# Kernel optimization log

Hardware: AMD Instinct MI355X
Metric: run time of the kernel (lower is better)

Reference implementation:

```python
import jax, jax.numpy as jnp
import numpy as np

B, N, D, H, L = 2, 1024, 256, 4, 6
DH = D // H          # head dim 64
RDIM = DH // 2       # AxialRotaryEmbedding dim = 32 -> output feature size DH
THETA = 0.01


def setup_inputs() -> dict:
    key = jax.random.key(0)
    ks = iter(jax.random.split(key, 80))
    def nrm(shape, s=1.0):
        return jax.random.normal(next(ks), shape, jnp.float32) * s
    size = jnp.array([1024.0, 768.0], jnp.float32)
    inp = {
        'kpts0': jax.random.uniform(next(ks), (B, N, 2), jnp.float32) * size,
        'kpts1': jax.random.uniform(next(ks), (B, N, 2), jnp.float32) * size,
        'desc0': nrm((B, N, D)),
        'desc1': nrm((B, N, D)),
        'fx': 1.0 / (THETA ** (jnp.arange(0, RDIM, 2, dtype=jnp.float32) / RDIM)),
        'fy': 1.0 / (THETA ** (jnp.arange(0, RDIM, 2, dtype=jnp.float32) / RDIM)),
    }
    s = D ** -0.5
    for p in ('s', 'c'):
        inp[f'{p}_Wqk'] = nrm((L, D, D), s); inp[f'{p}_bqk'] = jnp.zeros((L, D))
        inp[f'{p}_Wv'] = nrm((L, D, D), s);  inp[f'{p}_bv'] = jnp.zeros((L, D))
        inp[f'{p}_Wo'] = nrm((L, D, D), s);  inp[f'{p}_bo'] = jnp.zeros((L, D))
        inp[f'{p}_W1'] = nrm((L, 2 * D, 2 * D), (2 * D) ** -0.5); inp[f'{p}_b1'] = jnp.zeros((L, 2 * D))
        inp[f'{p}_g'] = jnp.ones((L, 2 * D)); inp[f'{p}_be'] = jnp.zeros((L, 2 * D))
        inp[f'{p}_W2'] = nrm((L, 2 * D, D), (2 * D) ** -0.5); inp[f'{p}_b2'] = jnp.zeros((L, D))
    inp['Wp'] = nrm((D, D), s); inp['bp'] = jnp.zeros((D,))
    inp['Wm'] = nrm((D, 1), s); inp['bm'] = jnp.zeros((1,))
    return inp


def reference(kpts0, kpts1, desc0, desc1, fx, fy,
              s_Wqk, s_bqk, s_Wv, s_bv, s_Wo, s_bo, s_W1, s_b1, s_g, s_be, s_W2, s_b2,
              c_Wqk, c_bqk, c_Wv, c_bv, c_Wo, c_bo, c_W1, c_b1, c_g, c_be, c_W2, c_b2,
              Wp, bp, Wm, bm):
    size = jnp.array([1024.0, 768.0], jnp.float32)
    norm_k = lambda k: (k - size / 2) / (size.max() / 2)
    heads = lambda t: t.reshape(t.shape[0], t.shape[1], H, DH)

    def rope(pos):  # pos [B,N,2] -> cos,sin [B,N,1,DH]
        f = jnp.concatenate([jnp.repeat(pos[..., 0:1] * fx, 2, -1),
                             jnp.repeat(pos[..., 1:2] * fy, 2, -1)], -1)[:, :, None, :]
        return jnp.cos(f), jnp.sin(f)

    def rot_half(x):  # pairs (x0,x1) -> (-x1,x0)
        return jnp.stack([-x[..., 1::2], x[..., 0::2]], -1).reshape(x.shape)

    def ln(x, g, b):
        mu = x.mean(-1, keepdims=True)
        v = ((x - mu) ** 2).mean(-1, keepdims=True)
        return (x - mu) / jnp.sqrt(v + 1e-5) * g + b

    def ffn(x, m, W1, b1, g, be, W2, b2):  # x + MLP(LN(concat(x,m)))
        h = jnp.concatenate([x, m], -1) @ W1 + b1
        return x + jax.nn.gelu(ln(h, g, be), approximate=False) @ W2 + b2

    cs0, sn0 = rope(norm_k(kpts0))
    cs1, sn1 = rope(norm_k(kpts1))
    x0, x1 = desc0, desc1
    for i in range(L):
        def self_blk(x, cs, sn):  # rotary self-attention, shared qk projection
            qk = heads(x @ s_Wqk[i] + s_bqk[i])
            qr = qk * cs + rot_half(qk) * sn
            v = heads(x @ s_Wv[i] + s_bv[i])
            a = jax.nn.softmax(jnp.einsum('bnhd,bmhd->bhnm', qr, qr) * DH ** -0.5, -1)
            m = jnp.einsum('bhnm,bmhd->bnhd', a, v).reshape(x.shape) @ s_Wo[i] + s_bo[i]
            return ffn(x, m, s_W1[i], s_b1[i], s_g[i], s_be[i], s_W2[i], s_b2[i])
        x0 = self_blk(x0, cs0, sn0)
        x1 = self_blk(x1, cs1, sn1)
        # bidirectional cross-attention (CrossTransformer math path)
        sc = (DH ** -0.5) ** 0.5
        qk0 = heads(x0 @ c_Wqk[i] + c_bqk[i]) * sc
        qk1 = heads(x1 @ c_Wqk[i] + c_bqk[i]) * sc
        v0 = heads(x0 @ c_Wv[i] + c_bv[i])
        v1 = heads(x1 @ c_Wv[i] + c_bv[i])
        sim = jnp.einsum('bnhd,bmhd->bhnm', qk0, qk1)
        m0 = jnp.einsum('bhnm,bmhd->bnhd', jax.nn.softmax(sim, -1), v1).reshape(x0.shape) @ c_Wo[i] + c_bo[i]
        m1 = jnp.einsum('bhnm,bnhd->bmhd', jax.nn.softmax(sim, 2), v0).reshape(x1.shape) @ c_Wo[i] + c_bo[i]
        x0 = ffn(x0, m0, c_W1[i], c_b1[i], c_g[i], c_be[i], c_W2[i], c_b2[i])
        x1 = ffn(x1, m1, c_W1[i], c_b1[i], c_g[i], c_be[i], c_W2[i], c_b2[i])
    # MatchAssignment: sigmoid log double softmax (temp=None, use_sqrt=False -> r=1)
    md0 = (x0 @ Wp + bp) / D ** 0.25
    md1 = (x1 @ Wp + bp) / D ** 0.25
    sim = jnp.einsum('bmd,bnd->bmn', md0, md1)
    z0 = x0 @ Wm + bm  # [B,N,1]
    z1 = x1 @ Wm + bm
    cert = jax.nn.log_sigmoid(z0) + jnp.swapaxes(jax.nn.log_sigmoid(z1), 1, 2)
    core = jax.nn.log_softmax(sim, -1) + jax.nn.log_softmax(sim, 1) + cert
    scores = jnp.zeros((sim.shape[0], N + 1, N + 1), sim.dtype)
    scores = scores.at[:, :N, :N].set(core)
    scores = scores.at[:, :N, N].set(jax.nn.log_sigmoid(-z0[..., 0]))
    scores = scores.at[:, N, :N].set(jax.nn.log_sigmoid(-z1[..., 0]))
    return scores
```

## Files before the change

### kernel.cpp

```cpp
#include <hip/hip_runtime.h>
#include <hip/hip_bf16.h>
#include <math.h>

#define NB 2
#define NN 1024
#define ND 256
#define NHD 4
#define NL 6
#define NP (NN + 1)

typedef unsigned short u16;
typedef __attribute__((ext_vector_type(8))) short bf16x8;
typedef __attribute__((ext_vector_type(4))) float f32x4;

__device__ __forceinline__ u16 f2b(float f) {
    union { float f; unsigned u; } v; v.f = f;
    unsigned r = v.u + 0x7FFFu + ((v.u >> 16) & 1u);
    return (u16)(r >> 16);
}
__device__ __forceinline__ float b2f(u16 b) {
    union { unsigned u; float f; } v; v.u = ((unsigned)b) << 16;
    return v.f;
}
__device__ __forceinline__ float logsigf(float x) {
    return (x >= 0.f) ? -log1pf(expf(-x)) : (x - log1pf(expf(x)));
}

__global__ void rope_cs_kernel(const float* __restrict__ kpts, const float* __restrict__ fx,
                               const float* __restrict__ fy, float* __restrict__ cs,
                               float* __restrict__ sn) {
    int idx = blockIdx.x * 256 + threadIdx.x;
    int row = idx >> 6, j = idx & 63;
    float kx = kpts[row * 2], ky = kpts[row * 2 + 1];
    float f;
    if (j < 32) f = ((kx - 512.f) * (1.f / 512.f)) * fx[j >> 1];
    else        f = ((ky - 384.f) * (1.f / 512.f)) * fy[(j - 32) >> 1];
    cs[idx] = cosf(f);
    sn[idx] = sinf(f);
}

__global__ void copyconv_kernel(const float* __restrict__ in, float* __restrict__ outf,
                                u16* __restrict__ outb, int n) {
    int i = blockIdx.x * 256 + threadIdx.x;
    if (i < n) { float v = in[i]; outf[i] = v; outb[i] = f2b(v); }
}

__global__ void wconv_kernel(const float* __restrict__ in, u16* __restrict__ out, int K, int N,
                             size_t outZ) {
    __shared__ float t[32][33];
    int z = blockIdx.z;
    int k0 = blockIdx.y * 32, n0 = blockIdx.x * 32;
    const float* W = in + (size_t)z * K * N;
    u16* Wt = out + (size_t)z * outZ;
    int tx = threadIdx.x, ty = threadIdx.y;
    for (int i = 0; i < 32; i += 8)
        t[ty + i][tx] = W[(size_t)(k0 + ty + i) * N + n0 + tx];
    __syncthreads();
    for (int i = 0; i < 32; i += 8)
        Wt[(size_t)(n0 + ty + i) * K + k0 + tx] = f2b(t[tx][ty + i]);
}

__global__ void biaspack_kernel(const float* __restrict__ b0, const float* __restrict__ b1,
                                float* __restrict__ out, int L) {
    int idx = blockIdx.x * 256 + threadIdx.x;
    if (idx >= L * 512) return;
    int i = idx >> 9, c = idx & 511;
    out[idx] = (c < 256) ? b0[i * 256 + c] : b1[i * 256 + c - 256];
}

__global__ __launch_bounds__(256)
void gemm_mfma(const u16* __restrict__ A, const u16* __restrict__ A2,
               const u16* __restrict__ Bt, const float* __restrict__ bias,
               const float* __restrict__ res, float* __restrict__ Cf, u16* __restrict__ Cb,
               int M, int N, int K, float scale_lo, float scale_hi,
               const float* __restrict__ csp, const float* __restrict__ snp) {
    __shared__ u16 As[2][64 * 72];
    __shared__ u16 Bs[2][64 * 72];
    int tid = threadIdx.x;
    int lane = tid & 63, wave = tid >> 6;
    int row0 = blockIdx.y * 64, col0 = blockIdx.x * 64;
    int wm = (wave >> 1) * 32, wn = (wave & 1) * 32;
    int l15 = lane & 15, l4 = lane >> 4;
    f32x4 acc[2][2] = {};
    int srl = tid >> 3, sc8 = (tid & 7) * 8;

    auto loadA = [&](int k0, int it) -> bf16x8 {
        int rr = row0 + srl + it * 32;
        int kg = k0 + sc8;
        const u16* src;
        if (A2) src = (kg < 256) ? &A[(size_t)rr * 256 + kg] : &A2[(size_t)rr * 256 + kg - 256];
        else    src = &A[(size_t)rr * K + kg];
        return *(const bf16x8*)src;
    };
    auto loadB = [&](int k0, int it) -> bf16x8 {
        return *(const bf16x8*)&Bt[(size_t)(col0 + srl + it * 32) * K + k0 + sc8];
    };

    bf16x8 rA0 = loadA(0, 0), rA1 = loadA(0, 1);
    bf16x8 rB0 = loadB(0, 0), rB1 = loadB(0, 1);
    *(bf16x8*)&As[0][srl * 72 + sc8] = rA0;
    *(bf16x8*)&As[0][(srl + 32) * 72 + sc8] = rA1;
    *(bf16x8*)&Bs[0][srl * 72 + sc8] = rB0;
    *(bf16x8*)&Bs[0][(srl + 32) * 72 + sc8] = rB1;
    __syncthreads();

    int nt = K >> 6;
    for (int t = 0; t < nt; ++t) {
        int buf = t & 1;
        bool more = (t + 1) < nt;
        if (more) {
            rA0 = loadA((t + 1) * 64, 0); rA1 = loadA((t + 1) * 64, 1);
            rB0 = loadB((t + 1) * 64, 0); rB1 = loadB((t + 1) * 64, 1);
        }
#pragma unroll
        for (int ks = 0; ks < 2; ++ks) {
            bf16x8 a0 = *(bf16x8*)&As[buf][(wm + l15) * 72 + ks * 32 + l4 * 8];
            bf16x8 a1 = *(bf16x8*)&As[buf][(wm + 16 + l15) * 72 + ks * 32 + l4 * 8];
            bf16x8 b0 = *(bf16x8*)&Bs[buf][(wn + l15) * 72 + ks * 32 + l4 * 8];
            bf16x8 b1 = *(bf16x8*)&Bs[buf][(wn + 16 + l15) * 72 + ks * 32 + l4 * 8];
            acc[0][0] = __builtin_amdgcn_mfma_f32_16x16x32_bf16(a0, b0, acc[0][0], 0, 0, 0);
            acc[0][1] = __builtin_amdgcn_mfma_f32_16x16x32_bf16(a0, b1, acc[0][1], 0, 0, 0);
            acc[1][0] = __builtin_amdgcn_mfma_f32_16x16x32_bf16(a1, b0, acc[1][0], 0, 0, 0);
            acc[1][1] = __builtin_amdgcn_mfma_f32_16x16x32_bf16(a1, b1, acc[1][1], 0, 0, 0);
        }
        if (more) {
            int nb = buf ^ 1;
            *(bf16x8*)&As[nb][srl * 72 + sc8] = rA0;
            *(bf16x8*)&As[nb][(srl + 32) * 72 + sc8] = rA1;
            *(bf16x8*)&Bs[nb][srl * 72 + sc8] = rB0;
            *(bf16x8*)&Bs[nb][(srl + 32) * 72 + sc8] = rB1;
        }
        __syncthreads();
    }
#pragma unroll
    for (int mi = 0; mi < 2; ++mi)
#pragma unroll
        for (int ni = 0; ni < 2; ++ni)
#pragma unroll
            for (int j = 0; j < 4; ++j) {
                int r = row0 + wm + mi * 16 + l4 * 4 + j;
                int c = col0 + wn + ni * 16 + l15;
                float v = acc[mi][ni][j] + (bias ? bias[c] : 0.f);
                float pn = __shfl_xor(v, 1);
                if (csp && c < 256) {
                    float cc = csp[(size_t)r * 64 + (c & 63)];
                    float ss = snp[(size_t)r * 64 + (c & 63)];
                    v = (c & 1) ? (v * cc + pn * ss) : (v * cc - pn * ss);
                }
                v *= (c < 256) ? scale_lo : scale_hi;
                if (res) v += res[(size_t)r * N + c];
                if (Cf) Cf[(size_t)r * N + c] = v;
                if (Cb) Cb[(size_t)r * N + c] = f2b(v);
            }
}

#define QSTR 72
#define VDSTR 1032
#define VBUFE (4 * VDSTR)

__global__ __launch_bounds__(256)
void flash_kernel(const u16* __restrict__ Qp, const u16* __restrict__ Vp,
                  u16* __restrict__ Ob, int kswap) {
    __shared__ u16 Qs[64 * QSTR];
    __shared__ u16 Ks[2][64 * QSTR];
    __shared__ u16 Vs[2][VBUFE];
    __shared__ u16 Ps[64 * QSTR];
    int y = blockIdx.y;
    int t = y >> 3, b = (y >> 2) & 1, h = y & 3;
    int qR = t * 2048 + b * 1024;
    int kt = kswap ? (1 - t) : t;
    int kR = kt * 2048 + b * 1024;
    int i0 = blockIdx.x * 64;
    int tid = threadIdx.x, lane = tid & 63, wave = tid >> 6;
    int l15 = lane & 15, l4 = lane >> 4;
    int wm = wave * 16;
    int srl = tid >> 3, sc8 = (tid & 7) * 8;

    const u16* Qbase = Qp + (size_t)(qR + i0) * 512 + h * 64;
    const u16* Kbase = Qp + (size_t)kR * 512 + h * 64;
    const u16* Vbase = Vp + (size_t)kR * 512 + h * 64;

#pragma unroll
    for (int it = 0; it < 2; ++it) {
        int rr = srl + it * 32;
        *(bf16x8*)&Qs[rr * QSTR + sc8] = *(const bf16x8*)&Qbase[(size_t)rr * 512 + sc8];
        *(bf16x8*)&Ks[0][rr * QSTR + sc8] = *(const bf16x8*)&Kbase[(size_t)rr * 512 + sc8];
        bf16x8 v = *(const bf16x8*)&Vbase[(size_t)rr * 512 + sc8];
        *(bf16x8*)&Vs[0][(sc8 >> 4) * VDSTR + rr * 16 + (sc8 & 15)] = v;
    }
    __syncthreads();

    float m[4], l[4];
    f32x4 accO[4] = {};
#pragma unroll
    for (int j = 0; j < 4; ++j) { m[j] = -1e30f; l[j] = 0.f; }

    for (int j0 = 0; j0 < NN; j0 += 64) {
        int buf = (j0 >> 6) & 1;
        bool more = (j0 + 64) < NN;
        bf16x8 nK0, nK1, nV0, nV1;
        if (more) {
            nK0 = *(const bf16x8*)&Kbase[(size_t)(j0 + 64 + srl) * 512 + sc8];
            nK1 = *(const bf16x8*)&Kbase[(size_t)(j0 + 96 + srl) * 512 + sc8];
            nV0 = *(const bf16x8*)&Vbase[(size_t)(j0 + 64 + srl) * 512 + sc8];
            nV1 = *(const bf16x8*)&Vbase[(size_t)(j0 + 96 + srl) * 512 + sc8];
        }
        f32x4 accS[4] = {};
#pragma unroll
        for (int ks = 0; ks < 2; ++ks) {
            bf16x8 a = *(bf16x8*)&Qs[(wm + l15) * QSTR + ks * 32 + l4 * 8];
#pragma unroll
            for (int n = 0; n < 4; ++n) {
                bf16x8 bb = *(bf16x8*)&Ks[buf][(n * 16 + l15) * QSTR + ks * 32 + l4 * 8];
                accS[n] = __builtin_amdgcn_mfma_f32_16x16x32_bf16(a, bb, accS[n], 0, 0, 0);
            }
        }
        float p[4][4];
#pragma unroll
        for (int j = 0; j < 4; ++j) {
            float tm = fmaxf(fmaxf(accS[0][j], accS[1][j]), fmaxf(accS[2][j], accS[3][j]));
#pragma unroll
            for (int d = 1; d < 16; d <<= 1) tm = fmaxf(tm, __shfl_xor(tm, d));
            float mnew = fmaxf(m[j], tm);
            float rr = __expf(m[j] - mnew);
            float ts = 0.f;
#pragma unroll
            for (int n = 0; n < 4; ++n) {
                float pv = __expf(accS[n][j] - mnew);
                p[n][j] = pv; ts += pv;
            }
#pragma unroll
            for (int d = 1; d < 16; d <<= 1) ts += __shfl_xor(ts, d);
            l[j] = l[j] * rr + ts;
            m[j] = mnew;
#pragma unroll
            for (int n = 0; n < 4; ++n) accO[n][j] *= rr;
        }
#pragma unroll
        for (int n = 0; n < 4; ++n) {
            int kv = n * 16 + l15;
            int c = (kv & 32) + (((kv >> 2) & 3) << 3) + (((kv >> 4) & 1) << 2) + (kv & 3);
#pragma unroll
            for (int j = 0; j < 4; ++j)
                Ps[(wm + l4 * 4 + j) * QSTR + c] = f2b(p[n][j]);
        }
#pragma unroll
        for (int ks = 0; ks < 2; ++ks) {
            bf16x8 a = *(bf16x8*)&Ps[(wm + l15) * QSTR + ks * 32 + l4 * 8];
#pragma unroll
            for (int n = 0; n < 4; ++n) {
                unsigned va = (unsigned)(size_t)(&Vs[buf][n * VDSTR]) + ks * 1024 + lane * 8;
                unsigned long long q0, q1;
                asm volatile("ds_read_b64_tr_b16 %0, %2\n\t"
                             "ds_read_b64_tr_b16 %1, %2 offset:512\n\t"
                             "s_waitcnt lgkmcnt(0)"
                             : "=&v"(q0), "=&v"(q1) : "v"(va) : "memory");
                union { unsigned long long q[2]; bf16x8 v; } uu;
                uu.q[0] = q0; uu.q[1] = q1;
                accO[n] = __builtin_amdgcn_mfma_f32_16x16x32_bf16(a, uu.v, accO[n], 0, 0, 0);
            }
        }
        if (more) {
            int nb = buf ^ 1;
            *(bf16x8*)&Ks[nb][srl * QSTR + sc8] = nK0;
            *(bf16x8*)&Ks[nb][(srl + 32) * QSTR + sc8] = nK1;
            *(bf16x8*)&Vs[nb][(sc8 >> 4) * VDSTR + srl * 16 + (sc8 & 15)] = nV0;
            *(bf16x8*)&Vs[nb][(sc8 >> 4) * VDSTR + (srl + 32) * 16 + (sc8 & 15)] = nV1;
        }
        __syncthreads();
    }
#pragma unroll
    for (int n = 0; n < 4; ++n)
#pragma unroll
        for (int j = 0; j < 4; ++j) {
            int r = i0 + wm + l4 * 4 + j;
            int d = n * 16 + l15;
            Ob[(size_t)(qR + r) * ND + h * 64 + d] = f2b(accO[n][j] / l[j]);
        }
}

__global__ void rowstats_kernel(const float* __restrict__ S, float* __restrict__ rm,
                                float* __restrict__ rs, int ncols) {
    __shared__ float sb[256];
    int row = blockIdx.x, tid = threadIdx.x;
    const float* p = S + (size_t)row * ncols;
    float m = -1e30f;
    for (int j = tid; j < ncols; j += 256) m = fmaxf(m, p[j]);
    sb[tid] = m; __syncthreads();
    for (int s = 128; s > 0; s >>= 1) { if (tid < s) sb[tid] = fmaxf(sb[tid], sb[tid + s]); __syncthreads(); }
    m = sb[0]; __syncthreads();
    float s = 0;
    for (int j = tid; j < ncols; j += 256) s += __expf(p[j] - m);
    sb[tid] = s; __syncthreads();
    for (int st = 128; st > 0; st >>= 1) { if (tid < st) sb[tid] += sb[tid + st]; __syncthreads(); }
    if (tid == 0) { rm[row] = m; rs[row] = sb[0]; }
}

#define CSCH 8
__global__ void colstats_part(const float* __restrict__ S, float* __restrict__ pm,
                              float* __restrict__ ps) {
    int mat = blockIdx.z;
    int j = blockIdx.x * 256 + threadIdx.x;
    int r0 = blockIdx.y * (NN / CSCH);
    const float* p = S + (size_t)mat * NN * NN + (size_t)r0 * NN + j;
    float m = -1e30f;
    for (int i = 0; i < NN / CSCH; ++i) m = fmaxf(m, p[(size_t)i * NN]);
    float s = 0;
    for (int i = 0; i < NN / CSCH; ++i) s += __expf(p[(size_t)i * NN] - m);
    int o = (mat * CSCH + blockIdx.y) * NN + j;
    pm[o] = m; ps[o] = s;
}
__global__ void colstats_red(const float* __restrict__ pm, const float* __restrict__ ps,
                             float* __restrict__ cm, float* __restrict__ cs) {
    int idx = blockIdx.x * 256 + threadIdx.x;
    int mat = idx >> 10, j = idx & 1023;
    float m = -1e30f;
#pragma unroll
    for (int k = 0; k < CSCH; ++k) m = fmaxf(m, pm[(mat * CSCH + k) * NN + j]);
    float s = 0;
#pragma unroll
    for (int k = 0; k < CSCH; ++k)
        s += ps[(mat * CSCH + k) * NN + j] * __expf(pm[(mat * CSCH + k) * NN + j] - m);
    cm[idx] = m; cs[idx] = s;
}

__global__ void ln_gelu_b(const u16* __restrict__ hb, const float* __restrict__ g,
                          const float* __restrict__ be, u16* __restrict__ out) {
    __shared__ float sb[256];
    int row = blockIdx.x, tid = threadIdx.x;
    const u16* p = hb + (size_t)row * 512;
    float x0 = b2f(p[tid]), x1 = b2f(p[tid + 256]);
    sb[tid] = x0 + x1; __syncthreads();
    for (int s = 128; s > 0; s >>= 1) { if (tid < s) sb[tid] += sb[tid + s]; __syncthreads(); }
    float mu = sb[0] * (1.f / 512.f); __syncthreads();
    float d0 = x0 - mu, d1 = x1 - mu;
    sb[tid] = d0 * d0 + d1 * d1; __syncthreads();
    for (int s = 128; s > 0; s >>= 1) { if (tid < s) sb[tid] += sb[tid + s]; __syncthreads(); }
    float rstd = rsqrtf(sb[0] * (1.f / 512.f) + 1e-5f);
    float y0 = d0 * rstd * g[tid] + be[tid];
    float y1 = d1 * rstd * g[tid + 256] + be[tid + 256];
    out[(size_t)row * 512 + tid]       = f2b(0.5f * y0 * (1.f + erff(y0 * 0.70710678118654752f)));
    out[(size_t)row * 512 + tid + 256] = f2b(0.5f * y1 * (1.f + erff(y1 * 0.70710678118654752f)));
}

__global__ void zproj_kernel(const float* __restrict__ X, const float* __restrict__ Wm,
                             const float* __restrict__ bm, float* __restrict__ z) {
    __shared__ float sb[256];
    int row = blockIdx.x, tid = threadIdx.x;
    float v = X[(size_t)row * 256 + tid] * Wm[tid];
    sb[tid] = v; __syncthreads();
    for (int s = 128; s > 0; s >>= 1) { if (tid < s) sb[tid] += sb[tid + s]; __syncthreads(); }
    if (tid == 0) z[row] = sb[0] + bm[0];
}

__global__ void assemble_kernel(const float* __restrict__ sim2, const float* __restrict__ z0,
                                const float* __restrict__ z1, const float* __restrict__ rm,
                                const float* __restrict__ rs, const float* __restrict__ cm,
                                const float* __restrict__ cs, float* __restrict__ out) {
    int idx = blockIdx.x * 256 + threadIdx.x;
    if (idx >= NB * NP * NP) return;
    int b = idx / (NP * NP);
    int rem = idx - b * NP * NP;
    int i = rem / NP, j = rem - i * NP;
    float v;
    if (i < NN && j < NN) {
        float s = sim2[((size_t)b * NN + i) * NN + j];
        float lr = s - rm[b * NN + i] - logf(rs[b * NN + i]);
        float lc = s - cm[b * NN + j] - logf(cs[b * NN + j]);
        v = lr + lc + logsigf(z0[b * NN + i]) + logsigf(z1[b * NN + j]);
    } else if (i < NN) {
        v = logsigf(-z0[b * NN + i]);
    } else if (j < NN) {
        v = logsigf(-z1[b * NN + j]);
    } else {
        v = 0.f;
    }
    out[idx] = v;
}

extern "C" void kernel_launch(void* const* d_in, const int* in_sizes, int n_in,
                              void* d_out, int out_size, void* d_ws, size_t ws_size,
                              hipStream_t stream) {
    auto in = [&](int i) { return (const float*)d_in[i]; };
    const float* kpts0 = in(0);
    const float* kpts1 = in(1);
    const float* desc0 = in(2);
    const float* desc1 = in(3);
    const float* fx = in(4);
    const float* fy = in(5);
    const float* sWqk = in(6);  const float* sbqk = in(7);
    const float* sWv  = in(8);  const float* sbv  = in(9);
    const float* sWo  = in(10); const float* sbo  = in(11);
    const float* sW1  = in(12); const float* sb1  = in(13);
    const float* sg   = in(14); const float* sbe  = in(15);
    const float* sW2  = in(16); const float* sb2  = in(17);
    const float* cWqk = in(18); const float* cbqk = in(19);
    const float* cWv  = in(20); const float* cbv  = in(21);
    const float* cWo  = in(22); const float* cbo  = in(23);
    const float* cW1  = in(24); const float* cb1  = in(25);
    const float* cg   = in(26); const float* cbe  = in(27);
    const float* cW2  = in(28); const float* cb2  = in(29);
    const float* Wp = in(30); const float* bp = in(31);
    const float* Wm = in(32); const float* bm = in(33);

    const int Mst = 2 * NB * NN;
    const size_t SND = (size_t)Mst * ND;

    char* base = (char*)d_ws;
    size_t off = 0;
    auto allocf = [&](size_t n) { float* p = (float*)(base + off); off += ((n * 4 + 255) & ~(size_t)255); return p; };
    auto allocb = [&](size_t n) { u16* p = (u16*)(base + off);   off += ((n * 2 + 255) & ~(size_t)255); return p; };

    float* x    = allocf(SND);
    float* cst  = allocf((size_t)Mst * 64);
    float* snt  = allocf((size_t)Mst * 64);
    float* simb = allocf((size_t)NB * NN * NN);
    float* z    = allocf(Mst);
    float* st0  = allocf(2048);
    float* st1  = allocf(2048);
    float* st2  = allocf(2048);
    float* st3  = allocf(2048);
    float* pm   = allocf((size_t)NB * CSCH * NN);
    float* ps   = allocf((size_t)NB * CSCH * NN);
    float* bqvs = allocf((size_t)NL * 512);
    float* bqvc = allocf((size_t)NL * 512);

    u16* xb    = allocb(SND);
    u16* tQVb  = allocb((size_t)Mst * 512);
    u16* attnb = allocb(SND);
    u16* mb    = allocb(SND);
    u16* hb    = allocb((size_t)Mst * 512);
    u16* hgb   = allocb((size_t)Mst * 512);
    u16* wsqv = allocb((size_t)NL * 512 * 256);
    u16* wso  = allocb((size_t)NL * 256 * 256);
    u16* wsw1 = allocb((size_t)NL * 512 * 512);
    u16* wsw2 = allocb((size_t)NL * 512 * 256);
    u16* wcqv = allocb((size_t)NL * 512 * 256);
    u16* wco  = allocb((size_t)NL * 256 * 256);
    u16* wcw1 = allocb((size_t)NL * 512 * 512);
    u16* wcw2 = allocb((size_t)NL * 512 * 256);
    u16* wpb  = allocb((size_t)256 * 256);

    auto wconv = [&](const float* w, u16* wt, int K, int N, int Lz, size_t outZ) {
        wconv_kernel<<<dim3(N / 32, K / 32, Lz), dim3(32, 8), 0, stream>>>(w, wt, K, N, outZ);
    };
    wconv(sWqk, wsqv,             256, 256, NL, 512 * 256);
    wconv(sWv,  wsqv + 256 * 256, 256, 256, NL, 512 * 256);
    wconv(cWqk, wcqv,             256, 256, NL, 512 * 256);
    wconv(cWv,  wcqv + 256 * 256, 256, 256, NL, 512 * 256);
    wconv(sWo, wso, 256, 256, NL, 256 * 256);
    wconv(cWo, wco, 256, 256, NL, 256 * 256);
    wconv(sW1, wsw1, 512, 512, NL, 512 * 512);
    wconv(cW1, wcw1, 512, 512, NL, 512 * 512);
    wconv(sW2, wsw2, 512, 256, NL, 512 * 256);
    wconv(cW2, wcw2, 512, 256, NL, 512 * 256);
    wconv(Wp, wpb, 256, 256, 1, 256 * 256);
    biaspack_kernel<<<(NL * 512 + 255) / 256, 256, 0, stream>>>(sbqk, sbv, bqvs, NL);
    biaspack_kernel<<<(NL * 512 + 255) / 256, 256, 0, stream>>>(cbqk, cbv, bqvc, NL);

    rope_cs_kernel<<<512, 256, 0, stream>>>(kpts0, fx, fy, cst, snt);
    rope_cs_kernel<<<512, 256, 0, stream>>>(kpts1, fx, fy, cst + 2048 * 64, snt + 2048 * 64);
    copyconv_kernel<<<2048, 256, 0, stream>>>(desc0, x, xb, (int)(SND / 2));
    copyconv_kernel<<<2048, 256, 0, stream>>>(desc1, x + SND / 2, xb + SND / 2, (int)(SND / 2));

    auto gemm = [&](const u16* A, const u16* A2, const u16* Bt, const float* bias,
                    const float* res, float* Cf, u16* Cb, int M, int N, int K,
                    float slo, float shi, const float* csp, const float* snp) {
        gemm_mfma<<<dim3(N / 64, M / 64), 256, 0, stream>>>(A, A2, Bt, bias, res, Cf, Cb,
                                                            M, N, K, slo, shi, csp, snp);
    };

    const float sc = 0.35355339059327379f;

    for (int i = 0; i < NL; ++i) {
        const size_t oQV = (size_t)i * 512 * 256;
        const size_t oDD = (size_t)i * 256 * 256;
        const size_t oW1 = (size_t)i * 512 * 512;
        const size_t oW2 = (size_t)i * 512 * 256;

        gemm(xb, nullptr, wsqv + oQV, bqvs + i * 512, nullptr, nullptr, tQVb,
             Mst, 512, 256, sc, 1.f, cst, snt);
        flash_kernel<<<dim3(16, 16), 256, 0, stream>>>(tQVb, tQVb + 256, attnb, 0);
        gemm(attnb, nullptr, wso + oDD, sbo + i * ND, nullptr, nullptr, mb,
             Mst, 256, 256, 1.f, 1.f, nullptr, nullptr);
        gemm(xb, mb, wsw1 + oW1, sb1 + i * 512, nullptr, nullptr, hb,
             Mst, 512, 512, 1.f, 1.f, nullptr, nullptr);
        ln_gelu_b<<<Mst, 256, 0, stream>>>(hb, sg + i * 512, sbe + i * 512, hgb);
        gemm(hgb, nullptr, wsw2 + oW2, sb2 + i * ND, x, x, xb,
             Mst, 256, 512, 1.f, 1.f, nullptr, nullptr);

        gemm(xb, nullptr, wcqv + oQV, bqvc + i * 512, nullptr, nullptr, tQVb,
             Mst, 512, 256, sc, 1.f, nullptr, nullptr);
        flash_kernel<<<dim3(16, 16), 256, 0, stream>>>(tQVb, tQVb + 256, attnb, 1);
        gemm(attnb, nullptr, wco + oDD, cbo + i * ND, nullptr, nullptr, mb,
             Mst, 256, 256, 1.f, 1.f, nullptr, nullptr);
        gemm(xb, mb, wcw1 + oW1, cb1 + i * 512, nullptr, nullptr, hb,
             Mst, 512, 512, 1.f, 1.f, nullptr, nullptr);
        ln_gelu_b<<<Mst, 256, 0, stream>>>(hb, cg + i * 512, cbe + i * 512, hgb);
        gemm(hgb, nullptr, wcw2 + oW2, cb2 + i * ND, x, x, xb,
             Mst, 256, 512, 1.f, 1.f, nullptr, nullptr);
    }

    gemm(xb, nullptr, wpb, bp, nullptr, nullptr, attnb,
         Mst, 256, 256, 0.25f, 0.25f, nullptr, nullptr);
    zproj_kernel<<<Mst, 256, 0, stream>>>(x, Wm, bm, z);
    for (int b = 0; b < NB; ++b) {
        gemm(attnb + (size_t)b * 1024 * 256, nullptr,
             attnb + (size_t)(2048 + b * 1024) * 256, nullptr, nullptr,
             simb + (size_t)b * NN * NN, nullptr,
             1024, 1024, 256, 1.f, 1.f, nullptr, nullptr);
    }
    rowstats_kernel<<<NB * NN, 256, 0, stream>>>(simb, st0, st1, NN);
    colstats_part<<<dim3(NN / 256, CSCH, NB), 256, 0, stream>>>(simb, pm, ps);
    colstats_red<<<(NB * NN) / 256, 256, 0, stream>>>(pm, ps, st2, st3);
    int total = NB * NP * NP;
    assemble_kernel<<<(total + 255) / 256, 256, 0, stream>>>(simb, z, z + 2048, st0, st1,
                                                             st2, st3, (float*)d_out);
}
```

Measured before the change: 1.185 ms.

## Split-K flash attention merged in O-proj GEMM, fuse LN+GELU into W2 GEMM

Flash attention now splits the key dimension into two halves, giving twice as many blocks, and writes unnormalized fp32 partial outputs plus per-row max and sum. The output-projection GEMM combines the two partials while loading its A operand. LayerNorm+GELU is folded into the W2 GEMM: per-row statistics are computed in the prologue and the activation is applied as each A tile is staged. Q fragments are hoisted into registers, and the weight-conversion, rope and copy setup kernels are merged into fewer launches. The trade-offs are extra fp32 partial traffic and redundant LN/GELU work in each column block of the W2 GEMM.

```diff
diff --git a/kernel.cpp b/kernel.cpp
--- a/kernel.cpp
+++ b/kernel.cpp
@@ -5,7 +5,6 @@
 #define NB 2
 #define NN 1024
 #define ND 256
-#define NHD 4
 #define NL 6
 #define NP (NN + 1)
 
@@ -26,12 +25,13 @@
     return (x >= 0.f) ? -log1pf(expf(-x)) : (x - log1pf(expf(x)));
 }
 
-__global__ void rope_cs_kernel(const float* __restrict__ kpts, const float* __restrict__ fx,
-                               const float* __restrict__ fy, float* __restrict__ cs,
-                               float* __restrict__ sn) {
+__global__ void rope_cs_kernel(const float* __restrict__ k0p, const float* __restrict__ k1p,
+                               const float* __restrict__ fx, const float* __restrict__ fy,
+                               float* __restrict__ cs, float* __restrict__ sn) {
     int idx = blockIdx.x * 256 + threadIdx.x;
     int row = idx >> 6, j = idx & 63;
-    float kx = kpts[row * 2], ky = kpts[row * 2 + 1];
+    const float* kp = (row < 2048) ? k0p + (size_t)row * 2 : k1p + (size_t)(row - 2048) * 2;
+    float kx = kp[0], ky = kp[1];
     float f;
     if (j < 32) f = ((kx - 512.f) * (1.f / 512.f)) * fx[j >> 1];
     else        f = ((ky - 384.f) * (1.f / 512.f)) * fy[(j - 32) >> 1];
@@ -39,19 +39,25 @@
     sn[idx] = sinf(f);
 }
 
-__global__ void copyconv_kernel(const float* __restrict__ in, float* __restrict__ outf,
-                                u16* __restrict__ outb, int n) {
+__global__ void copyconv_kernel(const float* __restrict__ d0, const float* __restrict__ d1,
+                                float* __restrict__ outf, u16* __restrict__ outb) {
     int i = blockIdx.x * 256 + threadIdx.x;
-    if (i < n) { float v = in[i]; outf[i] = v; outb[i] = f2b(v); }
-}
-
-__global__ void wconv_kernel(const float* __restrict__ in, u16* __restrict__ out, int K, int N,
-                             size_t outZ) {
+    float v = (i < 524288) ? d0[i] : d1[i - 524288];
+    outf[i] = v; outb[i] = f2b(v);
+}
+
+struct WP6 {
+    const float* s[6];
+    u16* d[6];
+    unsigned long long oz[6];
+};
+__global__ void wconvM_kernel(WP6 w, int perT, int K, int N) {
     __shared__ float t[32][33];
     int z = blockIdx.z;
+    int p = z / perT, l = z - p * perT;
+    const float* W = w.s[p] + (size_t)l * K * N;
+    u16* Wt = w.d[p] + (size_t)l * w.oz[p];
     int k0 = blockIdx.y * 32, n0 = blockIdx.x * 32;
-    const float* W = in + (size_t)z * K * N;
-    u16* Wt = out + (size_t)z * outZ;
     int tx = threadIdx.x, ty = threadIdx.y;
     for (int i = 0; i < 32; i += 8)
         t[ty + i][tx] = W[(size_t)(k0 + ty + i) * N + n0 + tx];
@@ -154,22 +160,219 @@
             }
 }
 
+__global__ __launch_bounds__(256)
+void gemm_oproj(const float* __restrict__ Op, const float* __restrict__ mp,
+                const float* __restrict__ lp, const u16* __restrict__ Bt,
+                const float* __restrict__ bias, u16* __restrict__ Cb) {
+    __shared__ u16 As[2][64 * 72];
+    __shared__ u16 Bs[2][64 * 72];
+    const int N = 256, K = 256;
+    int tid = threadIdx.x;
+    int lane = tid & 63, wave = tid >> 6;
+    int row0 = blockIdx.y * 64, col0 = blockIdx.x * 64;
+    int wm = (wave >> 1) * 32, wn = (wave & 1) * 32;
+    int l15 = lane & 15, l4 = lane >> 4;
+    f32x4 acc[2][2] = {};
+    int srl = tid >> 3, sc8 = (tid & 7) * 8;
+
+    auto loadA = [&](int k0, int it) -> bf16x8 {
+        int rg = row0 + srl + it * 32;
+        int kg = k0 + sc8;
+        int h = kg >> 6, d0 = kg & 63;
+        int t = rg >> 11, bb = (rg >> 10) & 1, iq = rg & 1023;
+        int y = t * 8 + bb * 4 + h;
+        int ri = y * 1024 + iq;
+        size_t base0 = (size_t)ri * 64 + d0;
+        size_t base1 = base0 + (size_t)16384 * 64;
+        f32x4 a0 = *(const f32x4*)&Op[base0];
+        f32x4 a1 = *(const f32x4*)&Op[base0 + 4];
+        f32x4 c0 = *(const f32x4*)&Op[base1];
+        f32x4 c1 = *(const f32x4*)&Op[base1 + 4];
+        float m0 = mp[ri], m1 = mp[16384 + ri];
+        float l0 = lp[ri], l1 = lp[16384 + ri];
+        float mf = fmaxf(m0, m1);
+        float e0 = __expf(m0 - mf), e1 = __expf(m1 - mf);
+        float inv = 1.f / (l0 * e0 + l1 * e1);
+        e0 *= inv; e1 *= inv;
+        u16 o[8];
+#pragma unroll
+        for (int e = 0; e < 4; ++e) {
+            o[e] = f2b(a0[e] * e0 + c0[e] * e1);
+            o[4 + e] = f2b(a1[e] * e0 + c1[e] * e1);
+        }
+        return *(bf16x8*)o;
+    };
+    auto loadB = [&](int k0, int it) -> bf16x8 {
+        return *(const bf16x8*)&Bt[(size_t)(col0 + srl + it * 32) * K + k0 + sc8];
+    };
+
+    bf16x8 rA0 = loadA(0, 0), rA1 = loadA(0, 1);
+    bf16x8 rB0 = loadB(0, 0), rB1 = loadB(0, 1);
+    *(bf16x8*)&As[0][srl * 72 + sc8] = rA0;
+    *(bf16x8*)&As[0][(srl + 32) * 72 + sc8] = rA1;
+    *(bf16x8*)&Bs[0][srl * 72 + sc8] = rB0;
+    *(bf16x8*)&Bs[0][(srl + 32) * 72 + sc8] = rB1;
+    __syncthreads();
+
+    for (int t = 0; t < 4; ++t) {
+        int buf = t & 1;
+        bool more = (t + 1) < 4;
+        if (more) {
+            rA0 = loadA((t + 1) * 64, 0); rA1 = loadA((t + 1) * 64, 1);
+            rB0 = loadB((t + 1) * 64, 0); rB1 = loadB((t + 1) * 64, 1);
+        }
+#pragma unroll
+        for (int ks = 0; ks < 2; ++ks) {
+            bf16x8 a0 = *(bf16x8*)&As[buf][(wm + l15) * 72 + ks * 32 + l4 * 8];
+            bf16x8 a1 = *(bf16x8*)&As[buf][(wm + 16 + l15) * 72 + ks * 32 + l4 * 8];
+            bf16x8 b0 = *(bf16x8*)&Bs[buf][(wn + l15) * 72 + ks * 32 + l4 * 8];
+            bf16x8 b1 = *(bf16x8*)&Bs[buf][(wn + 16 + l15) * 72 + ks * 32 + l4 * 8];
+            acc[0][0] = __builtin_amdgcn_mfma_f32_16x16x32_bf16(a0, b0, acc[0][0], 0, 0, 0);
+            acc[0][1] = __builtin_amdgcn_mfma_f32_16x16x32_bf16(a0, b1, acc[0][1], 0, 0, 0);
+            acc[1][0] = __builtin_amdgcn_mfma_f32_16x16x32_bf16(a1, b0, acc[1][0], 0, 0, 0);
+            acc[1][1] = __builtin_amdgcn_mfma_f32_16x16x32_bf16(a1, b1, acc[1][1], 0, 0, 0);
+        }
+        if (more) {
+            int nb = buf ^ 1;
+            *(bf16x8*)&As[nb][srl * 72 + sc8] = rA0;
+            *(bf16x8*)&As[nb][(srl + 32) * 72 + sc8] = rA1;
+            *(bf16x8*)&Bs[nb][srl * 72 + sc8] = rB0;
+            *(bf16x8*)&Bs[nb][(srl + 32) * 72 + sc8] = rB1;
+        }
+        __syncthreads();
+    }
+#pragma unroll
+    for (int mi = 0; mi < 2; ++mi)
+#pragma unroll
+        for (int ni = 0; ni < 2; ++ni)
+#pragma unroll
+            for (int j = 0; j < 4; ++j) {
+                int r = row0 + wm + mi * 16 + l4 * 4 + j;
+                int c = col0 + wn + ni * 16 + l15;
+                Cb[(size_t)r * N + c] = f2b(acc[mi][ni][j] + bias[c]);
+            }
+}
+
+__global__ __launch_bounds__(256)
+void gemm_w2ln(const u16* __restrict__ hb, const float* __restrict__ g,
+               const float* __restrict__ be, const u16* __restrict__ Bt,
+               const float* __restrict__ bias, float* __restrict__ xf,
+               u16* __restrict__ xb) {
+    __shared__ u16 As[2][64 * 72];
+    __shared__ u16 Bs[2][64 * 72];
+    __shared__ float muS[64], rsS[64];
+    const int N = 256, K = 512;
+    int tid = threadIdx.x;
+    int lane = tid & 63, wave = tid >> 6;
+    int row0 = blockIdx.y * 64, col0 = blockIdx.x * 64;
+    int wm = (wave >> 1) * 32, wn = (wave & 1) * 32;
+    int l15 = lane & 15, l4 = lane >> 4;
+    f32x4 acc[2][2] = {};
+
+    {
+        int rr = tid >> 2, seg = tid & 3;
+        const u16* hrow = hb + (size_t)(row0 + rr) * 512 + seg * 128;
+        float sum = 0.f, ss = 0.f;
+#pragma unroll
+        for (int q = 0; q < 16; ++q) {
+            bf16x8 v = *(const bf16x8*)&hrow[q * 8];
+#pragma unroll
+            for (int e = 0; e < 8; ++e) { float f = b2f(((u16*)&v)[e]); sum += f; ss += f * f; }
+        }
+        sum += __shfl_xor(sum, 1); ss += __shfl_xor(ss, 1);
+        sum += __shfl_xor(sum, 2); ss += __shfl_xor(ss, 2);
+        float mu = sum * (1.f / 512.f);
+        float var = ss * (1.f / 512.f) - mu * mu;
+        if (seg == 0) { muS[rr] = mu; rsS[rr] = rsqrtf(var + 1e-5f); }
+    }
+    __syncthreads();
+
+    int srl = tid >> 3, sc8 = (tid & 7) * 8;
+    auto ldA = [&](int k0, int it) -> bf16x8 {
+        return *(const bf16x8*)&hb[(size_t)(row0 + srl + it * 32) * 512 + k0 + sc8];
+    };
+    auto ldB = [&](int k0, int it) -> bf16x8 {
+        return *(const bf16x8*)&Bt[(size_t)(col0 + srl + it * 32) * K + k0 + sc8];
+    };
+    auto cook = [&](bf16x8 v, int it, int k0) -> bf16x8 {
+        int r = srl + it * 32;
+        float mu = muS[r], rs = rsS[r];
+        u16 o[8];
+#pragma unroll
+        for (int e = 0; e < 8; ++e) {
+            float y = (b2f(((u16*)&v)[e]) - mu) * rs * g[k0 + sc8 + e] + be[k0 + sc8 + e];
+            o[e] = f2b(0.5f * y * (1.f + erff(y * 0.70710678118654752f)));
+        }
+        return *(bf16x8*)o;
+    };
+
+    bf16x8 rA0 = ldA(0, 0), rA1 = ldA(0, 1);
+    bf16x8 rB0 = ldB(0, 0), rB1 = ldB(0, 1);
+    *(bf16x8*)&As[0][srl * 72 + sc8] = cook(rA0, 0, 0);
+    *(bf16x8*)&As[0][(srl + 32) * 72 + sc8] = cook(rA1, 1, 0);
+    *(bf16x8*)&Bs[0][srl * 72 + sc8] = rB0;
+    *(bf16x8*)&Bs[0][(srl + 32) * 72 + sc8] = rB1;
+    __syncthreads();
+
+    for (int t = 0; t < 8; ++t) {
+        int buf = t & 1;
+        bool more = (t + 1) < 8;
+        if (more) {
+            rA0 = ldA((t + 1) * 64, 0); rA1 = ldA((t + 1) * 64, 1);
+            rB0 = ldB((t + 1) * 64, 0); rB1 = ldB((t + 1) * 64, 1);
+        }
+#pragma unroll
+        for (int ks = 0; ks < 2; ++ks) {
+            bf16x8 a0 = *(bf16x8*)&As[buf][(wm + l15) * 72 + ks * 32 + l4 * 8];
+            bf16x8 a1 = *(bf16x8*)&As[buf][(wm + 16 + l15) * 72 + ks * 32 + l4 * 8];
+            bf16x8 b0 = *(bf16x8*)&Bs[buf][(wn + l15) * 72 + ks * 32 + l4 * 8];
+            bf16x8 b1 = *(bf16x8*)&Bs[buf][(wn + 16 + l15) * 72 + ks * 32 + l4 * 8];
+            acc[0][0] = __builtin_amdgcn_mfma_f32_16x16x32_bf16(a0, b0, acc[0][0], 0, 0, 0);
+            acc[0][1] = __builtin_amdgcn_mfma_f32_16x16x32_bf16(a0, b1, acc[0][1], 0, 0, 0);
+            acc[1][0] = __builtin_amdgcn_mfma_f32_16x16x32_bf16(a1, b0, acc[1][0], 0, 0, 0);
+            acc[1][1] = __builtin_amdgcn_mfma_f32_16x16x32_bf16(a1, b1, acc[1][1], 0, 0, 0);
+        }
+        if (more) {
+            int nb = buf ^ 1;
+            *(bf16x8*)&As[nb][srl * 72 + sc8] = cook(rA0, 0, (t + 1) * 64);
+            *(bf16x8*)&As[nb][(srl + 32) * 72 + sc8] = cook(rA1, 1, (t + 1) * 64);
+            *(bf16x8*)&Bs[nb][srl * 72 + sc8] = rB0;
+            *(bf16x8*)&Bs[nb][(srl + 32) * 72 + sc8] = rB1;
+        }
+        __syncthreads();
+    }
+#pragma unroll
+    for (int mi = 0; mi < 2; ++mi)
+#pragma unroll
+        for (int ni = 0; ni < 2; ++ni)
+#pragma unroll
+            for (int j = 0; j < 4; ++j) {
+                int r = row0 + wm + mi * 16 + l4 * 4 + j;
+                int c = col0 + wn + ni * 16 + l15;
+                float v = acc[mi][ni][j] + bias[c] + xf[(size_t)r * N + c];
+                xf[(size_t)r * N + c] = v;
+                xb[(size_t)r * N + c] = f2b(v);
+            }
+}
+
 #define QSTR 72
 #define VDSTR 1032
 #define VBUFE (4 * VDSTR)
 
 __global__ __launch_bounds__(256)
 void flash_kernel(const u16* __restrict__ Qp, const u16* __restrict__ Vp,
-                  u16* __restrict__ Ob, int kswap) {
+                  float* __restrict__ Op, float* __restrict__ mp, float* __restrict__ lp,
+                  int kswap) {
     __shared__ u16 Qs[64 * QSTR];
     __shared__ u16 Ks[2][64 * QSTR];
     __shared__ u16 Vs[2][VBUFE];
     __shared__ u16 Ps[64 * QSTR];
-    int y = blockIdx.y;
+    int y = blockIdx.z;
+    int half = blockIdx.y;
     int t = y >> 3, b = (y >> 2) & 1, h = y & 3;
     int qR = t * 2048 + b * 1024;
     int kt = kswap ? (1 - t) : t;
-    int kR = kt * 2048 + b * 1024;
+    int kR = kt * 2048 + b * 1024 + half * 512;
     int i0 = blockIdx.x * 64;
     int tid = threadIdx.x, lane = tid & 63, wave = tid >> 6;
     int l15 = lane & 15, l4 = lane >> 4;
@@ -190,14 +393,18 @@
     }
     __syncthreads();
 
+    bf16x8 qf[2];
+    qf[0] = *(bf16x8*)&Qs[(wm + l15) * QSTR + l4 * 8];
+    qf[1] = *(bf16x8*)&Qs[(wm + l15) * QSTR + 32 + l4 * 8];
+
     float m[4], l[4];
     f32x4 accO[4] = {};
 #pragma unroll
     for (int j = 0; j < 4; ++j) { m[j] = -1e30f; l[j] = 0.f; }
 
-    for (int j0 = 0; j0 < NN; j0 += 64) {
+    for (int j0 = 0; j0 < 512; j0 += 64) {
         int buf = (j0 >> 6) & 1;
-        bool more = (j0 + 64) < NN;
+        bool more = (j0 + 64) < 512;
         bf16x8 nK0, nK1, nV0, nV1;
         if (more) {
             nK0 = *(const bf16x8*)&Kbase[(size_t)(j0 + 64 + srl) * 512 + sc8];
@@ -208,11 +415,10 @@
         f32x4 accS[4] = {};
 #pragma unroll
         for (int ks = 0; ks < 2; ++ks) {
-            bf16x8 a = *(bf16x8*)&Qs[(wm + l15) * QSTR + ks * 32 + l4 * 8];
 #pragma unroll
             for (int n = 0; n < 4; ++n) {
                 bf16x8 bb = *(bf16x8*)&Ks[buf][(n * 16 + l15) * QSTR + ks * 32 + l4 * 8];
-                accS[n] = __builtin_amdgcn_mfma_f32_16x16x32_bf16(a, bb, accS[n], 0, 0, 0);
+                accS[n] = __builtin_amdgcn_mfma_f32_16x16x32_bf16(qf[ks], bb, accS[n], 0, 0, 0);
             }
         }
         float p[4][4];
@@ -269,14 +475,22 @@
         }
         __syncthreads();
     }
+    size_t obase = (size_t)(half * 16 + y) * 1024 + i0;
 #pragma unroll
     for (int n = 0; n < 4; ++n)
 #pragma unroll
         for (int j = 0; j < 4; ++j) {
-            int r = i0 + wm + l4 * 4 + j;
-            int d = n * 16 + l15;
-            Ob[(size_t)(qR + r) * ND + h * 64 + d] = f2b(accO[n][j] / l[j]);
-        }
+            int r = wm + l4 * 4 + j;
+            Op[(obase + r) * 64 + n * 16 + l15] = accO[n][j];
+        }
+    if (l15 == 0) {
+#pragma unroll
+        for (int j = 0; j < 4; ++j) {
+            int r = wm + l4 * 4 + j;
+            mp[obase + r] = m[j];
+            lp[obase + r] = l[j];
+        }
+    }
 }
 
 __global__ void rowstats_kernel(const float* __restrict__ S, float* __restrict__ rm,
@@ -322,25 +536,6 @@
     for (int k = 0; k < CSCH; ++k)
         s += ps[(mat * CSCH + k) * NN + j] * __expf(pm[(mat * CSCH + k) * NN + j] - m);
     cm[idx] = m; cs[idx] = s;
-}
-
-__global__ void ln_gelu_b(const u16* __restrict__ hb, const float* __restrict__ g,
-                          const float* __restrict__ be, u16* __restrict__ out) {
-    __shared__ float sb[256];
-    int row = blockIdx.x, tid = threadIdx.x;
-    const u16* p = hb + (size_t)row * 512;
-    float x0 = b2f(p[tid]), x1 = b2f(p[tid + 256]);
-    sb[tid] = x0 + x1; __syncthreads();
-    for (int s = 128; s > 0; s >>= 1) { if (tid < s) sb[tid] += sb[tid + s]; __syncthreads(); }
-    float mu = sb[0] * (1.f / 512.f); __syncthreads();
-    float d0 = x0 - mu, d1 = x1 - mu;
-    sb[tid] = d0 * d0 + d1 * d1; __syncthreads();
-    for (int s = 128; s > 0; s >>= 1) { if (tid < s) sb[tid] += sb[tid + s]; __syncthreads(); }
-    float rstd = rsqrtf(sb[0] * (1.f / 512.f) + 1e-5f);
-    float y0 = d0 * rstd * g[tid] + be[tid];
-    float y1 = d1 * rstd * g[tid + 256] + be[tid + 256];
-    out[(size_t)row * 512 + tid]       = f2b(0.5f * y0 * (1.f + erff(y0 * 0.70710678118654752f)));
-    out[(size_t)row * 512 + tid + 256] = f2b(0.5f * y1 * (1.f + erff(y1 * 0.70710678118654752f)));
 }
 
 __global__ void zproj_kernel(const float* __restrict__ X, const float* __restrict__ Wm,
@@ -415,13 +610,16 @@
     float* cst  = allocf((size_t)Mst * 64);
     float* snt  = allocf((size_t)Mst * 64);
     float* simb = allocf((size_t)NB * NN * NN);
+    float* Opb  = allocf((size_t)2 * 16384 * 64);
+    float* mpb  = allocf((size_t)2 * 16384);
+    float* lpb  = allocf((size_t)2 * 16384);
     float* z    = allocf(Mst);
     float* st0  = allocf(2048);
     float* st1  = allocf(2048);
     float* st2  = allocf(2048);
     float* st3  = allocf(2048);
-    float* pm   = allocf((size_t)NB * CSCH * NN);
-    float* ps   = allocf((size_t)NB * CSCH * NN);
+    float* pmb  = allocf((size_t)NB * CSCH * NN);
+    float* psb  = allocf((size_t)NB * CSCH * NN);
     float* bqvs = allocf((size_t)NL * 512);
     float* bqvc = allocf((size_t)NL * 512);
 
@@ -430,7 +628,6 @@
     u16* attnb = allocb(SND);
     u16* mb    = allocb(SND);
     u16* hb    = allocb((size_t)Mst * 512);
-    u16* hgb   = allocb((size_t)Mst * 512);
     u16* wsqv = allocb((size_t)NL * 512 * 256);
     u16* wso  = allocb((size_t)NL * 256 * 256);
     u16* wsw1 = allocb((size_t)NL * 512 * 512);
@@ -441,27 +638,32 @@
     u16* wcw2 = allocb((size_t)NL * 512 * 256);
     u16* wpb  = allocb((size_t)256 * 256);
 
-    auto wconv = [&](const float* w, u16* wt, int K, int N, int Lz, size_t outZ) {
-        wconv_kernel<<<dim3(N / 32, K / 32, Lz), dim3(32, 8), 0, stream>>>(w, wt, K, N, outZ);
-    };
-    wconv(sWqk, wsqv,             256, 256, NL, 512 * 256);
-    wconv(sWv,  wsqv + 256 * 256, 256, 256, NL, 512 * 256);
-    wconv(cWqk, wcqv,             256, 256, NL, 512 * 256);
-    wconv(cWv,  wcqv + 256 * 256, 256, 256, NL, 512 * 256);
-    wconv(sWo, wso, 256, 256, NL, 256 * 256);
-    wconv(cWo, wco, 256, 256, NL, 256 * 256);
-    wconv(sW1, wsw1, 512, 512, NL, 512 * 512);
-    wconv(cW1, wcw1, 512, 512, NL, 512 * 512);
-    wconv(sW2, wsw2, 512, 256, NL, 512 * 256);
-    wconv(cW2, wcw2, 512, 256, NL, 512 * 256);
-    wconv(Wp, wpb, 256, 256, 1, 256 * 256);
+    {
+        WP6 wa = {};
+        wa.s[0] = sWqk; wa.d[0] = wsqv;             wa.oz[0] = 512 * 256;
+        wa.s[1] = sWv;  wa.d[1] = wsqv + 256 * 256; wa.oz[1] = 512 * 256;
+        wa.s[2] = sWo;  wa.d[2] = wso;              wa.oz[2] = 256 * 256;
+        wa.s[3] = cWqk; wa.d[3] = wcqv;             wa.oz[3] = 512 * 256;
+        wa.s[4] = cWv;  wa.d[4] = wcqv + 256 * 256; wa.oz[4] = 512 * 256;
+        wa.s[5] = cWo;  wa.d[5] = wco;              wa.oz[5] = 256 * 256;
+        wconvM_kernel<<<dim3(8, 8, 36), dim3(32, 8), 0, stream>>>(wa, 6, 256, 256);
+        WP6 wb = {};
+        wb.s[0] = sW1; wb.d[0] = wsw1; wb.oz[0] = 512 * 512;
+        wb.s[1] = cW1; wb.d[1] = wcw1; wb.oz[1] = 512 * 512;
+        wconvM_kernel<<<dim3(16, 16, 12), dim3(32, 8), 0, stream>>>(wb, 6, 512, 512);
+        WP6 wc = {};
+        wc.s[0] = sW2; wc.d[0] = wsw2; wc.oz[0] = 512 * 256;
+        wc.s[1] = cW2; wc.d[1] = wcw2; wc.oz[1] = 512 * 256;
+        wconvM_kernel<<<dim3(8, 16, 12), dim3(32, 8), 0, stream>>>(wc, 6, 512, 256);
+        WP6 wd = {};
+        wd.s[0] = Wp; wd.d[0] = wpb; wd.oz[0] = 256 * 256;
+        wconvM_kernel<<<dim3(8, 8, 1), dim3(32, 8), 0, stream>>>(wd, 1, 256, 256);
+    }
     biaspack_kernel<<<(NL * 512 + 255) / 256, 256, 0, stream>>>(sbqk, sbv, bqvs, NL);
     biaspack_kernel<<<(NL * 512 + 255) / 256, 256, 0, stream>>>(cbqk, cbv, bqvc, NL);
 
-    rope_cs_kernel<<<512, 256, 0, stream>>>(kpts0, fx, fy, cst, snt);
-    rope_cs_kernel<<<512, 256, 0, stream>>>(kpts1, fx, fy, cst + 2048 * 64, snt + 2048 * 64);
-    copyconv_kernel<<<2048, 256, 0, stream>>>(desc0, x, xb, (int)(SND / 2));
-    copyconv_kernel<<<2048, 256, 0, stream>>>(desc1, x + SND / 2, xb + SND / 2, (int)(SND / 2));
+    rope_cs_kernel<<<1024, 256, 0, stream>>>(kpts0, kpts1, fx, fy, cst, snt);
+    copyconv_kernel<<<4096, 256, 0, stream>>>(desc0, desc1, x, xb);
 
     auto gemm = [&](const u16* A, const u16* A2, const u16* Bt, const float* bias,
                     const float* res, float* Cf, u16* Cb, int M, int N, int K,
@@ -480,25 +682,21 @@
 
         gemm(xb, nullptr, wsqv + oQV, bqvs + i * 512, nullptr, nullptr, tQVb,
              Mst, 512, 256, sc, 1.f, cst, snt);
-        flash_kernel<<<dim3(16, 16), 256, 0, stream>>>(tQVb, tQVb + 256, attnb, 0);
-        gemm(attnb, nullptr, wso + oDD, sbo + i * ND, nullptr, nullptr, mb,
-             Mst, 256, 256, 1.f, 1.f, nullptr, nullptr);
+        flash_kernel<<<dim3(16, 2, 16), 256, 0, stream>>>(tQVb, tQVb + 256, Opb, mpb, lpb, 0);
+        gemm_oproj<<<dim3(4, 64), 256, 0, stream>>>(Opb, mpb, lpb, wso + oDD, sbo + i * ND, mb);
         gemm(xb, mb, wsw1 + oW1, sb1 + i * 512, nullptr, nullptr, hb,
              Mst, 512, 512, 1.f, 1.f, nullptr, nullptr);
-        ln_gelu_b<<<Mst, 256, 0, stream>>>(hb, sg + i * 512, sbe + i * 512, hgb);
-        gemm(hgb, nullptr, wsw2 + oW2, sb2 + i * ND, x, x, xb,
-             Mst, 256, 512, 1.f, 1.f, nullptr, nullptr);
+        gemm_w2ln<<<dim3(4, 64), 256, 0, stream>>>(hb, sg + i * 512, sbe + i * 512,
+                                                   wsw2 + oW2, sb2 + i * ND, x, xb);
 
         gemm(xb, nullptr, wcqv + oQV, bqvc + i * 512, nullptr, nullptr, tQVb,
              Mst, 512, 256, sc, 1.f, nullptr, nullptr);
-        flash_kernel<<<dim3(16, 16), 256, 0, stream>>>(tQVb, tQVb + 256, attnb, 1);
-        gemm(attnb, nullptr, wco + oDD, cbo + i * ND, nullptr, nullptr, mb,
-             Mst, 256, 256, 1.f, 1.f, nullptr, nullptr);
+        flash_kernel<<<dim3(16, 2, 16), 256, 0, stream>>>(tQVb, tQVb + 256, Opb, mpb, lpb, 1);
+        gemm_oproj<<<dim3(4, 64), 256, 0, stream>>>(Opb, mpb, lpb, wco + oDD, cbo + i * ND, mb);
         gemm(xb, mb, wcw1 + oW1, cb1 + i * 512, nullptr, nullptr, hb,
              Mst, 512, 512, 1.f, 1.f, nullptr, nullptr);
-        ln_gelu_b<<<Mst, 256, 0, stream>>>(hb, cg + i * 512, cbe + i * 512, hgb);
-        gemm(hgb, nullptr, wcw2 + oW2, cb2 + i * ND, x, x, xb,
-             Mst, 256, 512, 1.f, 1.f, nullptr, nullptr);
+        gemm_w2ln<<<dim3(4, 64), 256, 0, stream>>>(hb, cg + i * 512, cbe + i * 512,
+                                                   wcw2 + oW2, cb2 + i * ND, x, xb);
     }
 
     gemm(xb, nullptr, wpb, bp, nullptr, nullptr, attnb,
@@ -511,8 +709,8 @@
              1024, 1024, 256, 1.f, 1.f, nullptr, nullptr);
     }
     rowstats_kernel<<<NB * NN, 256, 0, stream>>>(simb, st0, st1, NN);
-    colstats_part<<<dim3(NN / 256, CSCH, NB), 256, 0, stream>>>(simb, pm, ps);
-    colstats_red<<<(NB * NN) / 256, 256, 0, stream>>>(pm, ps, st2, st3);
+    colstats_part<<<dim3(NN / 256, CSCH, NB), 256, 0, stream>>>(simb, pmb, psb);
+    colstats_red<<<(NB * NN) / 256, 256, 0, stream>>>(pmb, psb, st2, st3);
     int total = NB * NP * NP;
     assemble_kernel<<<(total + 255) / 256, 256, 0, stream>>>(simb, z, z + 2048, st0, st1,
                                                              st2, st3, (float*)d_out);
```

Measured after the change: 1.205 ms. Within noise of the previous version (+1.7%).
